# Kernel optimization log

Measured on AMD Instinct MI355X. Metric: run time of the kernel, lower is better.

Reference implementation:

```python
import jax, jax.numpy as jnp
import numpy as np

INPUT_SHIFT = 0.1
K = 3  # extract_image_patches(x, 3) hardcodes 3x3 patches


def extract_image_patches(x, k):
    # x: [B, C, H, W] -> [B, k*k*C, Ho, Wo], patch ordering (kh, kw, C)
    B, C, H, W = x.shape
    Ho, Wo = H - k + 1, W - k + 1
    slices = [x[:, :, i:i + Ho, j:j + Wo] for i in range(k) for j in range(k)]
    return jnp.concatenate(slices, axis=1)


def smooth_max(z, axis):
    # SMorph smooth maximum: sum(z * softmax(z)) along axis
    w = jax.nn.softmax(z, axis=axis)
    return jnp.sum(z * w, axis=axis)


def _branch(logp, kflat):
    # logp: [B, P, Ho, Wo]; kflat: [P, O] -> [B, O, Ho, Wo]
    z = logp[:, :, None] + kflat[None, :, :, None, None]  # [B, P, O, Ho, Wo]
    return jnp.exp(smooth_max(z, axis=1))


def setup_inputs() -> dict:
    key = jax.random.key(0)
    kx, kk1, kk2 = jax.random.split(key, 3)
    B, C, H, W, O = 4, 32, 32, 32, 64
    fan_in = K * K * C
    fan_out = K * K * O
    limit = float(np.sqrt(6.0 / (fan_in + fan_out)))  # xavier_uniform
    x = jax.random.normal(kx, (B, C, H, W), dtype=jnp.float32)
    k1 = jax.random.uniform(kk1, (K, K, C, O), minval=-limit, maxval=limit, dtype=jnp.float32)
    k2 = jax.random.uniform(kk2, (K, K, C, O), minval=-limit, maxval=limit, dtype=jnp.float32)
    bias = jnp.zeros((O,), dtype=jnp.float32)
    return {"x": x, "k1": k1, "k2": k2, "bias": bias}


def reference(x, k1, k2, bias):
    kh, kw, C, O = k1.shape
    k1f = k1.reshape(kh * kw * C, O)
    k2f = k2.reshape(kh * kw * C, O)
    # log of clamped patches for +x and -x
    p1 = jnp.log(jnp.maximum(extract_image_patches(x, K), INPUT_SHIFT))
    p2 = jnp.log(jnp.maximum(extract_image_patches(-x, K), INPUT_SHIFT))
    y11 = _branch(p1, k1f)
    y12 = _branch(p1, k2f)
    y21 = _branch(p2, k1f)
    y22 = _branch(p2, k2f)
    return y11 - y12 - y21 + y22 + bias[None, :, None, None]
```

## Files before the change

### kernel.cpp

```cpp
#include <hip/hip_runtime.h>
#include <math.h>


typedef float  f32x4 __attribute__((ext_vector_type(4)));
typedef short  s16x8 __attribute__((ext_vector_type(8)));

#define BB   4
#define CC   32
#define HH   32
#define WW   32
#define OO   64
#define HO   30
#define WO   30
#define NSP  900
#define KDIM 576

#define T1   131072
#define T2   (T1 + 518400)
#define T3   (T2 + 18432)

__device__ __forceinline__ unsigned short f2bf(float f) {
    unsigned u = __float_as_uint(f);
    return (unsigned short)((u + 0x7FFFu + ((u >> 16) & 1u)) >> 16);
}

__global__ __launch_bounds__(256) void smorph_prep(
    const float* __restrict__ x, const float* __restrict__ k1,
    const float* __restrict__ k2, float4* __restrict__ pixs,
    uint4* __restrict__ A3, unsigned short* __restrict__ bt)
{
    const int t = blockIdx.x * 256 + threadIdx.x;

    if (t < T1) {
        const int pix = t >> 5, c = t & 31;
        const int b = pix >> 10, h = (pix >> 5) & 31, w = pix & 31;
        float v = x[b*32768 + c*1024 + h*32 + w];
        float mp = fmaxf(v, 0.1f), mn = fmaxf(-v, 0.1f);
        float lp = mp * logf(mp), ln_ = mn * logf(mn);
        float s0 = mp, s1 = lp, s2 = mn, s3 = ln_;
#pragma unroll
        for (int m = 16; m >= 1; m >>= 1) {
            s0 += __shfl_xor(s0, m); s1 += __shfl_xor(s1, m);
            s2 += __shfl_xor(s2, m); s3 += __shfl_xor(s3, m);
        }
        if (c == 0) pixs[pix] = make_float4(s0, s1, s2, s3);
    } else if (t < T2) {
        const int u   = t - T1;
        const int mt  = u / 2304, rem = u - mt*2304;
        const int st  = rem >> 7, rem2 = rem & 127;
        const int mi  = rem2 >> 6, l = rem2 & 63;
        const int lr  = l & 15, lg = l >> 4;
        const int s   = mt*16 + mi*8 + (lr >> 1);
        const int sign = lr & 1;
        const int pos = st >> 1, khalf = st & 1;
        const int kh  = pos / 3, kw = pos - 3*(pos/3);
        const int b   = s / NSP, r = s - b*NSP;
        const int ho  = r / WO,  wo = r - WO*(r/WO);
        const int h   = ho + kh, w = wo + kw;
        const int c0  = khalf*16 + lg*4;
        const int base = b*32768 + h*32 + w;
        unsigned pk[4];
#pragma unroll
        for (int q = 0; q < 4; ++q) {
            float v = x[base + (c0 + q)*1024];
            float m = sign ? fmaxf(-v, 0.1f) : fmaxf(v, 0.1f);
            pk[q] = (unsigned)f2bf(m) | ((unsigned)f2bf(m * logf(m)) << 16);
        }
        A3[u] = make_uint4(pk[0], pk[1], pk[2], pk[3]);
    } else if (t < T3) {
        const int u3 = t - T2;
        const int o = u3 & 63, p = u3 >> 6;
        const float a = k1[u3], b2 = k2[u3];
        const float d1 = expm1f(a),  q1 = a  * expf(a);
        const float d2 = expm1f(b2), q2 = b2 * expf(b2);
        const float vals[4][2] = {{d1, 0.f}, {q1, d1}, {d2, 0.f}, {q2, d2}};
#pragma unroll
        for (int tbl = 0; tbl < 4; ++tbl) {
            const int n = o*4 + tbl;
#pragma unroll
            for (int ks = 0; ks < 2; ++ks) {
                const int k    = 2*p + ks;
                const int st   = k >> 5, k32 = k & 31;
                const int lane = (n & 15) + ((k32 >> 3) << 4);
                bt[((n >> 4)*18 + st)*512 + lane*8 + (k32 & 7)] = f2bf(vals[tbl][ks]);
            }
        }
    }
}

__global__ __launch_bounds__(128) void smorph_gemm(
    const uint4* __restrict__ A3, const unsigned short* __restrict__ bt,
    const float4* __restrict__ pixs, const float* __restrict__ bias,
    float* __restrict__ out)
{
    __shared__ __align__(16) float lds[2][32*66];

    const int tid = threadIdx.x;
    const int l   = tid & 63;
    const int w   = tid >> 6;
    const int bm  = blockIdx.x >> 1;
    const int nh  = blockIdx.x & 1;
    const int N0  = nh*128 + w*64;
    const int ng0 = N0 >> 4;

    const int lr = l & 15;
    const int lg = l >> 4;

    float4 S;
    {
        const int s  = bm*16 + lr;
        const int b  = s / NSP, r = s - b*NSP;
        const int ho = r / WO,  wo = r - WO*(r/WO);
        const float4* P = pixs + (b*1024 + ho*32 + wo);
        float4 acc = make_float4(0,0,0,0);
#pragma unroll
        for (int kh = 0; kh < 3; ++kh)
#pragma unroll
            for (int kw = 0; kw < 3; ++kw) {
                float4 v = P[kh*32 + kw];
                acc.x += v.x; acc.y += v.y; acc.z += v.z; acc.w += v.w;
            }
        S = acc;
    }

    const uint4* Ap = A3 + ((size_t)bm*18)*128 + l;
    const char*  pb = (const char*)bt;

    f32x4 acc[2][4] = {};

#pragma unroll
    for (int step = 0; step < 18; ++step) {
        s16x8 a0 = *(const s16x8*)(Ap + (step*2 + 0)*64);
        s16x8 a1 = *(const s16x8*)(Ap + (step*2 + 1)*64);
        s16x8 b0 = *(const s16x8*)(pb + (((ng0+0)*18 + step)*64 + l)*16);
        s16x8 b1 = *(const s16x8*)(pb + (((ng0+1)*18 + step)*64 + l)*16);
        s16x8 b2 = *(const s16x8*)(pb + (((ng0+2)*18 + step)*64 + l)*16);
        s16x8 b3 = *(const s16x8*)(pb + (((ng0+3)*18 + step)*64 + l)*16);

        acc[0][0] = __builtin_amdgcn_mfma_f32_16x16x32_bf16(a0, b0, acc[0][0], 0, 0, 0);
        acc[0][1] = __builtin_amdgcn_mfma_f32_16x16x32_bf16(a0, b1, acc[0][1], 0, 0, 0);
        acc[0][2] = __builtin_amdgcn_mfma_f32_16x16x32_bf16(a0, b2, acc[0][2], 0, 0, 0);
        acc[0][3] = __builtin_amdgcn_mfma_f32_16x16x32_bf16(a0, b3, acc[0][3], 0, 0, 0);
        acc[1][0] = __builtin_amdgcn_mfma_f32_16x16x32_bf16(a1, b0, acc[1][0], 0, 0, 0);
        acc[1][1] = __builtin_amdgcn_mfma_f32_16x16x32_bf16(a1, b1, acc[1][1], 0, 0, 0);
        acc[1][2] = __builtin_amdgcn_mfma_f32_16x16x32_bf16(a1, b2, acc[1][2], 0, 0, 0);
        acc[1][3] = __builtin_amdgcn_mfma_f32_16x16x32_bf16(a1, b3, acc[1][3], 0, 0, 0);
    }

    {
        float* L = &lds[w][0];
        const int wrbase = lg*4*66 + lr;
#pragma unroll
        for (int mi = 0; mi < 2; ++mi)
#pragma unroll
            for (int ni = 0; ni < 4; ++ni)
#pragma unroll
                for (int r = 0; r < 4; ++r)
                    L[wrbase + (mi*16 + r)*66 + ni*16] = acc[mi][ni][r];
    }
    __syncthreads();

    {
        const int sl = lr;
        const int oq = lg;
        const int s  = bm*16 + sl;
        const int b  = s / NSP;
        const int r900 = s - b*NSP;
        const float* Lw = &lds[w][0];
#pragma unroll
        for (int oi = 0; oi < 4; ++oi) {
            int ol = oq*4 + oi;
            int o  = (N0 >> 2) + ol;
            float4 v0 = *(const float4*)&Lw[(2*sl + 0)*66 + ol*4];
            float4 v1 = *(const float4*)&Lw[(2*sl + 1)*66 + ol*4];
            float d1p = S.x + v0.x, n1p = S.y + v0.y;
            float d2p = S.x + v0.z, n2p = S.y + v0.w;
            float d1n = S.z + v1.x, n1n = S.w + v1.y;
            float d2n = S.z + v1.z, n2n = S.w + v1.w;
            float P = __expf(n1p/d1p) - __expf(n2p/d2p)
                    - __expf(n1n/d1n) + __expf(n2n/d2n);
            out[((size_t)(b*OO + o))*NSP + r900] = P + bias[o];
        }
    }
}

extern "C" void kernel_launch(void* const* d_in, const int* in_sizes, int n_in,
                              void* d_out, int out_size, void* d_ws, size_t ws_size,
                              hipStream_t stream) {
    const float* x    = (const float*)d_in[0];
    const float* k1   = (const float*)d_in[1];
    const float* k2   = (const float*)d_in[2];
    const float* bias = (const float*)d_in[3];

    char* ws = (char*)d_ws;
    float4*         pixs = (float4*)(ws);
    uint4*          A3   = (uint4*)(ws + 0x10000);
    unsigned short* bt   = (unsigned short*)(ws + 0x7F9000);
    float*          out  = (float*)d_out;

    hipLaunchKernelGGL(smorph_prep, dim3(T3/256), dim3(256), 0, stream,
                       x, k1, k2, pixs, A3, bt);
    hipLaunchKernelGGL(smorph_gemm, dim3(450), dim3(128), 0, stream,
                       A3, bt, pixs, bias, out);
}
```

Baseline: 21.50 us.

## Split GEMM K-loop across two wave pairs with LDS reduction; use fast log

The GEMM block grows from 2 to 4 waves. Each pair of waves takes half of the 18 K-steps, and the partial accumulators are summed through shared memory before the epilogue. This adds more waves for latency hiding on a small 450-block grid. It costs an extra LDS round trip and a barrier, and half the waves sit idle during the epilogue. The prep kernel also swaps logf for __logf, trading a little precision for cheaper transcendentals.

```diff
diff --git a/kernel.cpp b/kernel.cpp
--- a/kernel.cpp
+++ b/kernel.cpp
@@ -64,7 +64,7 @@
         for (int q = 0; q < 4; ++q) {
             float v = x[base + (c0 + q)*1024];
             float m = sign ? fmaxf(-v, 0.1f) : fmaxf(v, 0.1f);
-            pk[q] = (unsigned)f2bf(m) | ((unsigned)f2bf(m * logf(m)) << 16);
+            pk[q] = (unsigned)f2bf(m) | ((unsigned)f2bf(m * __logf(m)) << 16);
         }
         A3[u] = make_uint4(pk[0], pk[1], pk[2], pk[3]);
     } else if (t < T3) {
@@ -88,19 +88,22 @@
     }
 }
 
-__global__ __launch_bounds__(128) void smorph_gemm(
+__global__ __launch_bounds__(256, 2) void smorph_gemm(
     const uint4* __restrict__ A3, const unsigned short* __restrict__ bt,
     const float4* __restrict__ pixs, const float* __restrict__ bias,
     float* __restrict__ out)
 {
-    __shared__ __align__(16) float lds[2][32*66];
+    __shared__ float cmb[2][2048];
+    __shared__ __align__(16) float epi[2][32*66];
 
     const int tid = threadIdx.x;
     const int l   = tid & 63;
     const int w   = tid >> 6;
+    const int kq  = w >> 1;
+    const int nhf = w & 1;
     const int bm  = blockIdx.x >> 1;
     const int nh  = blockIdx.x & 1;
-    const int N0  = nh*128 + w*64;
+    const int N0  = nh*128 + nhf*64;
     const int ng0 = N0 >> 4;
 
     const int lr = l & 15;
@@ -112,15 +115,15 @@
         const int b  = s / NSP, r = s - b*NSP;
         const int ho = r / WO,  wo = r - WO*(r/WO);
         const float4* P = pixs + (b*1024 + ho*32 + wo);
-        float4 acc = make_float4(0,0,0,0);
+        float4 a = make_float4(0,0,0,0);
 #pragma unroll
         for (int kh = 0; kh < 3; ++kh)
 #pragma unroll
             for (int kw = 0; kw < 3; ++kw) {
                 float4 v = P[kh*32 + kw];
-                acc.x += v.x; acc.y += v.y; acc.z += v.z; acc.w += v.w;
+                a.x += v.x; a.y += v.y; a.z += v.z; a.w += v.w;
             }
-        S = acc;
+        S = a;
     }
 
     const uint4* Ap = A3 + ((size_t)bm*18)*128 + l;
@@ -129,7 +132,8 @@
     f32x4 acc[2][4] = {};
 
 #pragma unroll
-    for (int step = 0; step < 18; ++step) {
+    for (int s2 = 0; s2 < 9; ++s2) {
+        const int step = s2*2 + kq;
         s16x8 a0 = *(const s16x8*)(Ap + (step*2 + 0)*64);
         s16x8 a1 = *(const s16x8*)(Ap + (step*2 + 1)*64);
         s16x8 b0 = *(const s16x8*)(pb + (((ng0+0)*18 + step)*64 + l)*16);
@@ -147,8 +151,25 @@
         acc[1][3] = __builtin_amdgcn_mfma_f32_16x16x32_bf16(a1, b3, acc[1][3], 0, 0, 0);
     }
 
-    {
-        float* L = &lds[w][0];
+    if (kq == 1) {
+#pragma unroll
+        for (int mi = 0; mi < 2; ++mi)
+#pragma unroll
+            for (int ni = 0; ni < 4; ++ni)
+#pragma unroll
+                for (int r = 0; r < 4; ++r)
+                    cmb[nhf][(mi*16 + ni*4 + r)*64 + l] = acc[mi][ni][r];
+    }
+    __syncthreads();
+    if (kq == 0) {
+#pragma unroll
+        for (int mi = 0; mi < 2; ++mi)
+#pragma unroll
+            for (int ni = 0; ni < 4; ++ni)
+#pragma unroll
+                for (int r = 0; r < 4; ++r)
+                    acc[mi][ni][r] += cmb[nhf][(mi*16 + ni*4 + r)*64 + l];
+
         const int wrbase = lg*4*66 + lr;
 #pragma unroll
         for (int mi = 0; mi < 2; ++mi)
@@ -156,23 +177,22 @@
             for (int ni = 0; ni < 4; ++ni)
 #pragma unroll
                 for (int r = 0; r < 4; ++r)
-                    L[wrbase + (mi*16 + r)*66 + ni*16] = acc[mi][ni][r];
+                    epi[nhf][wrbase + (mi*16 + r)*66 + ni*16] = acc[mi][ni][r];
     }
     __syncthreads();
 
-    {
+    if (kq == 0) {
         const int sl = lr;
         const int oq = lg;
         const int s  = bm*16 + sl;
         const int b  = s / NSP;
         const int r900 = s - b*NSP;
-        const float* Lw = &lds[w][0];
 #pragma unroll
         for (int oi = 0; oi < 4; ++oi) {
             int ol = oq*4 + oi;
             int o  = (N0 >> 2) + ol;
-            float4 v0 = *(const float4*)&Lw[(2*sl + 0)*66 + ol*4];
-            float4 v1 = *(const float4*)&Lw[(2*sl + 1)*66 + ol*4];
+            float4 v0 = *(const float4*)&epi[nhf][(2*sl + 0)*66 + ol*4];
+            float4 v1 = *(const float4*)&epi[nhf][(2*sl + 1)*66 + ol*4];
             float d1p = S.x + v0.x, n1p = S.y + v0.y;
             float d2p = S.x + v0.z, n2p = S.y + v0.w;
             float d1n = S.z + v1.x, n1n = S.w + v1.y;
@@ -198,8 +218,8 @@
     unsigned short* bt   = (unsigned short*)(ws + 0x7F9000);
     float*          out  = (float*)d_out;
 
-    hipLaunchKernelGGL(smorph_prep, dim3(T3/256), dim3(256), 0, stream,
+    hipLaunchKernelGGL(smorph_prep, dim3((T3 + 255)/256), dim3(256), 0, stream,
                        x, k1, k2, pixs, A3, bt);
-    hipLaunchKernelGGL(smorph_gemm, dim3(450), dim3(128), 0, stream,
+    hipLaunchKernelGGL(smorph_gemm, dim3(450), dim3(256), 0, stream,
                        A3, bt, pixs, bias, out);
 }
```

New measurement: 20.78 us. -3.3%, faster.
